# Kernel optimization log

Measured on AMD Instinct MI355X. Metric: run time of the kernel, lower is better.

Reference implementation:

```python
import jax, jax.numpy as jnp
import numpy as np

NUM_HEADS = 16
HEAD_SIZE = 64
N_EMBED = 1024
BLOCK_SIZE = 1024
BATCH = 8


def setup_inputs() -> dict:
    key = jax.random.key(0)
    ks = jax.random.split(key, 8)
    s_in = 1.0 / np.sqrt(N_EMBED)
    x = jax.random.normal(ks[0], (BATCH, BLOCK_SIZE, N_EMBED), dtype=jnp.float32)
    Wq = jax.random.normal(ks[1], (N_EMBED, N_EMBED), dtype=jnp.float32) * s_in
    Wk = jax.random.normal(ks[2], (N_EMBED, N_EMBED), dtype=jnp.float32) * s_in
    Wv = jax.random.normal(ks[3], (N_EMBED, N_EMBED), dtype=jnp.float32) * s_in
    Wo = jax.random.normal(ks[4], (N_EMBED, N_EMBED), dtype=jnp.float32) * s_in
    bo = jnp.zeros((N_EMBED,), dtype=jnp.float32)
    W1 = jax.random.normal(ks[5], (N_EMBED, N_EMBED), dtype=jnp.float32) * s_in
    b1 = jnp.zeros((N_EMBED,), dtype=jnp.float32)
    return {"x": x, "Wq": Wq, "Wk": Wk, "Wv": Wv, "Wo": Wo, "bo": bo, "W1": W1, "b1": b1}


def reference(x, Wq, Wk, Wv, Wo, bo, W1, b1):
    B, T, E = x.shape
    H, Dh = NUM_HEADS, HEAD_SIZE
    # per-head projections (bias=False), concatenated weights reshaped to heads
    q = (x @ Wq).reshape(B, T, H, Dh)
    k = (x @ Wk).reshape(B, T, H, Dh)
    v = (x @ Wv).reshape(B, T, H, Dh)
    scale = Dh ** -0.5
    scores = jnp.einsum("bqhd,bkhd->bhqk", q, k) * scale  # [B,H,T,T]
    causal = jnp.tril(jnp.ones((T, T), dtype=bool))
    scores = jnp.where(causal, scores, jnp.float32(-jnp.inf))
    attn = jax.nn.softmax(scores, axis=-1)
    out = jnp.einsum("bhqk,bkhd->bqhd", attn, v).reshape(B, T, E)
    out = out @ Wo + bo  # output projection
    # FeedForward: Linear(E, E) + ReLU
    out = jax.nn.relu(out @ W1 + b1)
    return out
```

## Files before the change

kernel.cpp:

```cpp
#include <hip/hip_runtime.h>

typedef __bf16 bf16x8 __attribute__((ext_vector_type(8)));
typedef float f32x4 __attribute__((ext_vector_type(4)));
typedef short short4v __attribute__((ext_vector_type(4)));
typedef short short8v __attribute__((ext_vector_type(8)));

#define DEVI static __device__ __forceinline__

DEVI short f2bf(float f) {
    union { __bf16 b; short s; } u;
    u.b = (__bf16)f;
    return u.s;
}

DEVI void gld16(const void* g, void* l) {
    __builtin_amdgcn_global_load_lds(
        (const __attribute__((address_space(1))) unsigned int*)g,
        (__attribute__((address_space(3))) unsigned int*)l, 16, 0, 0);
}

__global__ __launch_bounds__(256) void cvt_x_kernel(const float* __restrict__ x,
                                                    short* __restrict__ xb) {
    int i = (blockIdx.x * 256 + threadIdx.x) * 8;
    f32x4 a = *(const f32x4*)(x + i);
    f32x4 b = *(const f32x4*)(x + i + 4);
    short8v o;
    o[0]=f2bf(a[0]); o[1]=f2bf(a[1]); o[2]=f2bf(a[2]); o[3]=f2bf(a[3]);
    o[4]=f2bf(b[0]); o[5]=f2bf(b[1]); o[6]=f2bf(b[2]); o[7]=f2bf(b[3]);
    *(short8v*)(xb + i) = o;
}

__global__ __launch_bounds__(256) void wtrans5_kernel(const float* __restrict__ w0,
                                                      const float* __restrict__ w1,
                                                      const float* __restrict__ w2,
                                                      const float* __restrict__ w3,
                                                      const float* __restrict__ w4,
                                                      short* __restrict__ dst) {
    const float* w;
    switch (blockIdx.z) {
        case 0: w = w0; break;
        case 1: w = w1; break;
        case 2: w = w2; break;
        case 3: w = w3; break;
        default: w = w4; break;
    }
    short* wt = dst + (size_t)blockIdx.z * 1048576;
    __shared__ float t[64][68];
    const int tid = threadIdx.x;
    const int k0 = blockIdx.x * 64, n0 = blockIdx.y * 64;
#pragma unroll
    for (int it = 0; it < 4; ++it) {
        int r = (tid >> 4) + it * 16;
        int cc = (tid & 15) * 4;
        f32x4 vv = *(const f32x4*)(w + (k0 + r) * 1024 + n0 + cc);
        *(f32x4*)&t[r][cc] = vv;
    }
    __syncthreads();
#pragma unroll
    for (int it = 0; it < 4; ++it) {
        int n = (tid >> 4) + it * 16;
        int kc = (tid & 15) * 4;
        short4v o;
        o[0] = f2bf(t[kc + 0][n]);
        o[1] = f2bf(t[kc + 1][n]);
        o[2] = f2bf(t[kc + 2][n]);
        o[3] = f2bf(t[kc + 3][n]);
        *(short4v*)(wt + (n0 + n) * 1024 + k0 + kc) = o;
    }
}

template<int MODE>
__global__ __launch_bounds__(256, 2) void gemm_bt(const short* __restrict__ A,
                                                  const short* __restrict__ Bt,
                                                  const float* __restrict__ bias,
                                                  void* __restrict__ outp) {
    __shared__ short As[128 * 64];
    __shared__ short Bs[128 * 64];
    const int tid = threadIdx.x;
    const int lane = tid & 63;
    const int wid = tid >> 6;
    const int g = lane >> 4, c = lane & 15;
    const int wr = wid >> 1, wc = wid & 1;
    const int m0 = blockIdx.x * 128, n0 = blockIdx.y * 128;

    const f32x4 fz = {0.f, 0.f, 0.f, 0.f};
    f32x4 acc[4][4];
#pragma unroll
    for (int m = 0; m < 4; ++m)
#pragma unroll
        for (int n = 0; n < 4; ++n) acc[m][n] = fz;

    for (int kt = 0; kt < 16; ++kt) {
        const int k0 = kt * 64;
        __syncthreads();
#pragma unroll
        for (int st = 0; st < 4; ++st) {
            int ci = st * 256 + tid;
            int r = ci >> 3;
            int cc = ((ci & 7) ^ (r & 7)) << 3;
            gld16(A + (m0 + r) * 1024 + k0 + cc, (char*)As + ci * 16);
            gld16(Bt + (n0 + r) * 1024 + k0 + cc, (char*)Bs + ci * 16);
        }
        __syncthreads();
#pragma unroll
        for (int kk = 0; kk < 2; ++kk) {
            bf16x8 af[4], bfr[4];
#pragma unroll
            for (int m = 0; m < 4; ++m) {
                int row = wr * 64 + m * 16 + c;
                af[m] = *(const bf16x8*)((const char*)As + row * 128 + ((kk * 64 + g * 16) ^ ((row & 7) << 4)));
            }
#pragma unroll
            for (int n = 0; n < 4; ++n) {
                int row = wc * 64 + n * 16 + c;
                bfr[n] = *(const bf16x8*)((const char*)Bs + row * 128 + ((kk * 64 + g * 16) ^ ((row & 7) << 4)));
            }
#pragma unroll
            for (int m = 0; m < 4; ++m)
#pragma unroll
                for (int n = 0; n < 4; ++n)
                    acc[m][n] = __builtin_amdgcn_mfma_f32_16x16x32_bf16(af[m], bfr[n], acc[m][n], 0, 0, 0);
        }
    }

#pragma unroll
    for (int n = 0; n < 4; ++n) {
        const int col = n0 + wc * 64 + n * 16 + c;
        float bv = 0.f;
        if (MODE != 0) bv = bias[col];
#pragma unroll
        for (int m = 0; m < 4; ++m) {
            const int row0 = m0 + wr * 64 + m * 16 + g * 4;
#pragma unroll
            for (int i = 0; i < 4; ++i) {
                const int row = row0 + i;
                float val = acc[m][n][i];
                if (MODE == 0) {
                    short* qkv = (short*)outp;
                    int which = col >> 10;
                    int hc = col & 1023;
                    int dst = which * 8388608 +
                              (((row >> 10) * 16 + (hc >> 6)) * 1024 + (row & 1023)) * 64 + (hc & 63);
                    qkv[dst] = f2bf(val);
                } else if (MODE == 1) {
                    ((short*)outp)[row * 1024 + col] = f2bf(val + bv);
                } else {
                    ((float*)outp)[row * 1024 + col] = fmaxf(val + bv, 0.f);
                }
            }
        }
    }
}

__global__ __launch_bounds__(512, 2) void attn_kernel(const short* __restrict__ qp,
                                                      const short* __restrict__ kp,
                                                      const short* __restrict__ vp,
                                                      short* __restrict__ ao) {
    __shared__ short Ks[128 * 64];
    __shared__ short Vt[64 * 128];
    __shared__ short Ps[8][16 * 64];
    const float SCALE = 0.125f * 1.44269504088896340736f;
    const int tid = threadIdx.x;
    const int lane = tid & 63;
    const int wid = tid >> 6;
    const int g = lane >> 4, c = lane & 15;
    const int bh = blockIdx.y;
    const int base = bh * 65536;
    const int b = bh >> 4, h = bh & 15;

    const int r0 = tid >> 3, c0 = (tid & 7) << 3;
    const int r1 = 64 + r0;
    const int vt0 = (tid >> 4) * 4;
    const int vd0 = (tid & 15) * 4;

    const f32x4 fz = {0.f, 0.f, 0.f, 0.f};

    bf16x8 kreg0, kreg1;
    short4v vreg0, vreg1, vreg2, vreg3;

#pragma unroll 1
    for (int ph = 0; ph < 2; ++ph) {
        const int qt = ph ? (7 - blockIdx.x) : blockIdx.x;
        const int q0 = qt * 128;
        const int nkt = qt + 1;

        const int qrow = q0 + wid * 16 + c;
        bf16x8 qf0 = *(const bf16x8*)(qp + base + qrow * 64 + g * 8);
        bf16x8 qf1 = *(const bf16x8*)(qp + base + qrow * 64 + 32 + g * 8);

        f32x4 accO[4];
#pragma unroll
        for (int n = 0; n < 4; ++n) accO[n] = fz;
        float mrow[4], lsum[4];
#pragma unroll
        for (int i = 0; i < 4; ++i) { mrow[i] = -1e30f; lsum[i] = 0.f; }

        kreg0 = *(const bf16x8*)(kp + base + r0 * 64 + c0);
        kreg1 = *(const bf16x8*)(kp + base + r1 * 64 + c0);
        vreg0 = *(const short4v*)(vp + base + (vt0 + 0) * 64 + vd0);
        vreg1 = *(const short4v*)(vp + base + (vt0 + 1) * 64 + vd0);
        vreg2 = *(const short4v*)(vp + base + (vt0 + 2) * 64 + vd0);
        vreg3 = *(const short4v*)(vp + base + (vt0 + 3) * 64 + vd0);

        for (int kt = 0; kt < nkt; ++kt) {
            __syncthreads();
            *(bf16x8*)((char*)Ks + r0 * 128 + ((c0 * 2) ^ ((r0 & 7) << 4))) = kreg0;
            *(bf16x8*)((char*)Ks + r1 * 128 + ((c0 * 2) ^ ((r1 & 7) << 4))) = kreg1;
#pragma unroll
            for (int i = 0; i < 4; ++i) {
                short4v w; w[0] = vreg0[i]; w[1] = vreg1[i]; w[2] = vreg2[i]; w[3] = vreg3[i];
                int d = vd0 + i;
                int swz = ((d & 7) ^ (d >> 3)) << 4;
                *(short4v*)((char*)Vt + d * 256 + ((vt0 * 2) ^ swz)) = w;
            }
            if (kt + 1 < nkt) {
                const short* kp2 = kp + base + (kt + 1) * 8192;
                const short* vp2 = vp + base + (kt + 1) * 8192;
                kreg0 = *(const bf16x8*)(kp2 + r0 * 64 + c0);
                kreg1 = *(const bf16x8*)(kp2 + r1 * 64 + c0);
                vreg0 = *(const short4v*)(vp2 + (vt0 + 0) * 64 + vd0);
                vreg1 = *(const short4v*)(vp2 + (vt0 + 1) * 64 + vd0);
                vreg2 = *(const short4v*)(vp2 + (vt0 + 2) * 64 + vd0);
                vreg3 = *(const short4v*)(vp2 + (vt0 + 3) * 64 + vd0);
            }
            __syncthreads();

            const bool diag = (kt == nkt - 1);
            const int nlim = diag ? (wid + 1) : 8;

            f32x4 s[8];
            __builtin_amdgcn_s_setprio(1);
#pragma unroll
            for (int n = 0; n < 8; ++n) {
                s[n] = fz;
                if (n < nlim) {
                    int row = n * 16 + c;
                    int swz = (row & 7) << 4;
                    bf16x8 kf0 = *(const bf16x8*)((const char*)Ks + row * 128 + ((g * 16) ^ swz));
                    bf16x8 kf1 = *(const bf16x8*)((const char*)Ks + row * 128 + ((64 + g * 16) ^ swz));
                    s[n] = __builtin_amdgcn_mfma_f32_16x16x32_bf16(qf0, kf0, s[n], 0, 0, 0);
                    s[n] = __builtin_amdgcn_mfma_f32_16x16x32_bf16(qf1, kf1, s[n], 0, 0, 0);
                }
            }
            __builtin_amdgcn_s_setprio(0);

            const int qg0 = q0 + wid * 16 + g * 4;
            float pm[4];
#pragma unroll
            for (int i = 0; i < 4; ++i) pm[i] = -1e30f;
            if (diag) {
#pragma unroll
                for (int n = 0; n < 8; ++n) {
                    int kg = kt * 128 + n * 16 + c;
#pragma unroll
                    for (int i = 0; i < 4; ++i) {
                        float vv = s[n][i] * SCALE;
                        vv = (kg <= qg0 + i) ? vv : -1e30f;
                        s[n][i] = vv;
                        pm[i] = fmaxf(pm[i], vv);
                    }
                }
            } else {
#pragma unroll
                for (int n = 0; n < 8; ++n)
#pragma unroll
                    for (int i = 0; i < 4; ++i) {
                        float vv = s[n][i] * SCALE;
                        s[n][i] = vv;
                        pm[i] = fmaxf(pm[i], vv);
                    }
            }
#pragma unroll
            for (int off = 1; off < 16; off <<= 1)
#pragma unroll
                for (int i = 0; i < 4; ++i)
                    pm[i] = fmaxf(pm[i], __shfl_xor(pm[i], off));

            int need = 0;
#pragma unroll
            for (int i = 0; i < 4; ++i) need |= (pm[i] > mrow[i] + 8.f) ? 1 : 0;
            if (__any(need)) {
#pragma unroll
                for (int i = 0; i < 4; ++i) {
                    float mnew = fmaxf(mrow[i], pm[i]);
                    float corr = exp2f(mrow[i] - mnew);
                    mrow[i] = mnew;
                    lsum[i] *= corr;
#pragma unroll
                    for (int n = 0; n < 4; ++n) accO[n][i] *= corr;
                }
            }
#pragma unroll
            for (int n = 0; n < 8; ++n)
#pragma unroll
                for (int i = 0; i < 4; ++i) {
                    float pv = exp2f(s[n][i] - mrow[i]);
                    s[n][i] = pv;
                    lsum[i] += pv;
                }

#pragma unroll
            for (int hf = 0; hf < 2; ++hf) {
                asm volatile("s_waitcnt lgkmcnt(0)" ::: "memory");
                __builtin_amdgcn_sched_barrier(0);
#pragma unroll
                for (int n4 = 0; n4 < 4; ++n4) {
                    int tl = n4 * 16 + c;
#pragma unroll
                    for (int i = 0; i < 4; ++i) {
                        int q = g * 4 + i;
                        *(short*)((char*)&Ps[wid][0] + q * 128 + ((tl * 2) ^ ((q & 7) << 4))) =
                            f2bf(s[hf * 4 + n4][i]);
                    }
                }
                asm volatile("s_waitcnt lgkmcnt(0)" ::: "memory");
                __builtin_amdgcn_sched_barrier(0);
#pragma unroll
                for (int ksl = 0; ksl < 2; ++ksl) {
                    const int ks = hf * 2 + ksl;
                    bf16x8 paf = *(const bf16x8*)((const char*)&Ps[wid][0] +
                                                  c * 128 + ((ksl * 64 + g * 16) ^ ((c & 7) << 4)));
                    __builtin_amdgcn_s_setprio(1);
#pragma unroll
                    for (int n = 0; n < 4; ++n) {
                        int d = n * 16 + c;
                        int swz = ((d & 7) ^ (d >> 3)) << 4;
                        bf16x8 vf = *(const bf16x8*)((const char*)Vt + d * 256 + ((ks * 64 + g * 16) ^ swz));
                        accO[n] = __builtin_amdgcn_mfma_f32_16x16x32_bf16(paf, vf, accO[n], 0, 0, 0);
                    }
                    __builtin_amdgcn_s_setprio(0);
                }
            }
        }

        float lrow[4];
#pragma unroll
        for (int i = 0; i < 4; ++i) lrow[i] = lsum[i];
#pragma unroll
        for (int off = 1; off < 16; off <<= 1)
#pragma unroll
            for (int i = 0; i < 4; ++i)
                lrow[i] += __shfl_xor(lrow[i], off);
        float inv[4];
#pragma unroll
        for (int i = 0; i < 4; ++i) inv[i] = __builtin_amdgcn_rcpf(lrow[i]);
#pragma unroll
        for (int n = 0; n < 4; ++n)
#pragma unroll
            for (int i = 0; i < 4; ++i) {
                int t = q0 + wid * 16 + g * 4 + i;
                float o = accO[n][i] * inv[i];
                ao[(b * 1024 + t) * 1024 + h * 64 + n * 16 + c] = f2bf(o);
            }
    }
}

extern "C" void kernel_launch(void* const* d_in, const int* in_sizes, int n_in,
                              void* d_out, int out_size, void* d_ws, size_t ws_size,
                              hipStream_t stream) {
    const float* x  = (const float*)d_in[0];
    const float* Wq = (const float*)d_in[1];
    const float* Wk = (const float*)d_in[2];
    const float* Wv = (const float*)d_in[3];
    const float* Wo = (const float*)d_in[4];
    const float* bo = (const float*)d_in[5];
    const float* W1 = (const float*)d_in[6];
    const float* b1 = (const float*)d_in[7];

    char* ws = (char*)d_ws;
    short* xb    = (short*)(ws + 0);
    short* wallT = (short*)(ws + 16777216);
    short* qb    = (short*)(ws + 27262976);
    short* kb    = qb + 8388608;
    short* vb    = qb + 16777216;
    short* ao    = xb;
    short* o2    = qb;
    short* wqkvT = wallT;
    short* woT   = wallT + 3145728;
    short* w1T   = wallT + 4194304;

    cvt_x_kernel<<<4096, 256, 0, stream>>>(x, xb);
    wtrans5_kernel<<<dim3(16, 16, 5), 256, 0, stream>>>(Wq, Wk, Wv, Wo, W1, wallT);

    gemm_bt<0><<<dim3(64, 24), 256, 0, stream>>>(xb, wqkvT, nullptr, (void*)qb);
    attn_kernel<<<dim3(4, 128), 512, 0, stream>>>(qb, kb, vb, ao);
    gemm_bt<1><<<dim3(64, 8), 256, 0, stream>>>(ao, woT, bo, (void*)o2);
    gemm_bt<2><<<dim3(64, 8), 256, 0, stream>>>(o2, w1T, b1, d_out);
}
```

Baseline: 173.8 us.

## Fold Wo and W1 into one combined weight and pre-scale Q

Since there is no nonlinearity between the output projection and the FFN linear layer, the change precomputes Wcomb = Wo·W1 with a small 1024x1024 GEMM and a combined bias b1 + bo·W1. That removes one full 8192x1024x1024 activation GEMM and its intermediate round trip through memory. It also folds the softmax scale (with the log2e factor) into Q at QKV projection time, dropping the per-score multiply in attention. The cost is an extra rounding of the combined weight to bf16, plus a serial bias kernel that loops over 1024 rows per thread.

Measured after the change: 219.3 us. 1.26x slower.

```diff
diff --git a/kernel.cpp b/kernel.cpp
--- a/kernel.cpp
+++ b/kernel.cpp
@@ -56,17 +56,42 @@
         *(f32x4*)&t[r][cc] = vv;
     }
     __syncthreads();
-#pragma unroll
-    for (int it = 0; it < 4; ++it) {
-        int n = (tid >> 4) + it * 16;
-        int kc = (tid & 15) * 4;
-        short4v o;
-        o[0] = f2bf(t[kc + 0][n]);
-        o[1] = f2bf(t[kc + 1][n]);
-        o[2] = f2bf(t[kc + 2][n]);
-        o[3] = f2bf(t[kc + 3][n]);
-        *(short4v*)(wt + (n0 + n) * 1024 + k0 + kc) = o;
-    }
+    if (blockIdx.z == 3) {
+#pragma unroll
+        for (int it = 0; it < 4; ++it) {
+            int r = (tid >> 4) + it * 16;
+            int cc = (tid & 15) * 4;
+            short4v o;
+            o[0] = f2bf(t[r][cc + 0]);
+            o[1] = f2bf(t[r][cc + 1]);
+            o[2] = f2bf(t[r][cc + 2]);
+            o[3] = f2bf(t[r][cc + 3]);
+            *(short4v*)(wt + (k0 + r) * 1024 + n0 + cc) = o;
+        }
+    } else {
+#pragma unroll
+        for (int it = 0; it < 4; ++it) {
+            int n = (tid >> 4) + it * 16;
+            int kc = (tid & 15) * 4;
+            short4v o;
+            o[0] = f2bf(t[kc + 0][n]);
+            o[1] = f2bf(t[kc + 1][n]);
+            o[2] = f2bf(t[kc + 2][n]);
+            o[3] = f2bf(t[kc + 3][n]);
+            *(short4v*)(wt + (n0 + n) * 1024 + k0 + kc) = o;
+        }
+    }
+}
+
+__global__ __launch_bounds__(256) void bcomb_kernel(const float* __restrict__ bo,
+                                                    const float* __restrict__ W1,
+                                                    const float* __restrict__ b1,
+                                                    float* __restrict__ out) {
+    int n = blockIdx.x * 256 + threadIdx.x;
+    float acc = b1[n];
+    for (int j = 0; j < 1024; ++j)
+        acc += bo[j] * W1[j * 1024 + n];
+    out[n] = acc;
 }
 
 template<int MODE>
@@ -127,7 +152,7 @@
     for (int n = 0; n < 4; ++n) {
         const int col = n0 + wc * 64 + n * 16 + c;
         float bv = 0.f;
-        if (MODE != 0) bv = bias[col];
+        if (MODE == 2) bv = bias[col];
 #pragma unroll
         for (int m = 0; m < 4; ++m) {
             const int row0 = m0 + wr * 64 + m * 16 + g * 4;
@@ -139,13 +164,14 @@
                     short* qkv = (short*)outp;
                     int which = col >> 10;
                     int hc = col & 1023;
+                    if (which == 0) val *= 0.18033688011112042f;
                     int dst = which * 8388608 +
                               (((row >> 10) * 16 + (hc >> 6)) * 1024 + (row & 1023)) * 64 + (hc & 63);
                     qkv[dst] = f2bf(val);
-                } else if (MODE == 1) {
-                    ((short*)outp)[row * 1024 + col] = f2bf(val + bv);
+                } else if (MODE == 2) {
+                    ((float*)outp)[row * 1024 + col] = fmaxf(val + bv, 0.f);
                 } else {
-                    ((float*)outp)[row * 1024 + col] = fmaxf(val + bv, 0.f);
+                    ((short*)outp)[row * 1024 + col] = f2bf(val);
                 }
             }
         }
@@ -159,7 +185,6 @@
     __shared__ short Ks[128 * 64];
     __shared__ short Vt[64 * 128];
     __shared__ short Ps[8][16 * 64];
-    const float SCALE = 0.125f * 1.44269504088896340736f;
     const int tid = threadIdx.x;
     const int lane = tid & 63;
     const int wid = tid >> 6;
@@ -254,7 +279,7 @@
                     int kg = kt * 128 + n * 16 + c;
 #pragma unroll
                     for (int i = 0; i < 4; ++i) {
-                        float vv = s[n][i] * SCALE;
+                        float vv = s[n][i];
                         vv = (kg <= qg0 + i) ? vv : -1e30f;
                         s[n][i] = vv;
                         pm[i] = fmaxf(pm[i], vv);
@@ -264,11 +289,8 @@
 #pragma unroll
                 for (int n = 0; n < 8; ++n)
 #pragma unroll
-                    for (int i = 0; i < 4; ++i) {
-                        float vv = s[n][i] * SCALE;
-                        s[n][i] = vv;
-                        pm[i] = fmaxf(pm[i], vv);
-                    }
+                    for (int i = 0; i < 4; ++i)
+                        pm[i] = fmaxf(pm[i], s[n][i]);
             }
 #pragma unroll
             for (int off = 1; off < 16; off <<= 1)
@@ -374,16 +396,20 @@
     short* kb    = qb + 8388608;
     short* vb    = qb + 16777216;
     short* ao    = xb;
-    short* o2    = qb;
     short* wqkvT = wallT;
-    short* woT   = wallT + 3145728;
+    short* woBF  = wallT + 3145728;
     short* w1T   = wallT + 4194304;
+    short* wcombT= wqkvT;
+    float* bcomb = (float*)(ws + 16777216 + 2097152 * 4);
+
+    bcomb = (float*)(ws + 16777216 + 2097152);
 
     cvt_x_kernel<<<4096, 256, 0, stream>>>(x, xb);
     wtrans5_kernel<<<dim3(16, 16, 5), 256, 0, stream>>>(Wq, Wk, Wv, Wo, W1, wallT);
 
     gemm_bt<0><<<dim3(64, 24), 256, 0, stream>>>(xb, wqkvT, nullptr, (void*)qb);
+    gemm_bt<3><<<dim3(8, 8), 256, 0, stream>>>(w1T, woBF, nullptr, (void*)wcombT);
+    bcomb_kernel<<<4, 256, 0, stream>>>(bo, W1, b1, bcomb);
     attn_kernel<<<dim3(4, 128), 512, 0, stream>>>(qb, kb, vb, ao);
-    gemm_bt<1><<<dim3(64, 8), 256, 0, stream>>>(ao, woT, bo, (void*)o2);
-    gemm_bt<2><<<dim3(64, 8), 256, 0, stream>>>(o2, w1T, b1, d_out);
-}
+    gemm_bt<2><<<dim3(64, 8), 256, 0, stream>>>(ao, wcombT, bcomb, d_out);
+}
```
